# Kernel optimization log

Hardware: AMD Instinct MI355X
Metric: run time of the kernel (lower is better)

Reference implementation:

```python
import jax, jax.numpy as jnp
import numpy as np

B, S, D, H = 2, 2048, 1024, 16
DK = D // H
ROPE_BASE = 10000.0


def _rope_tables(seq_len, dim):
    # [S, dim] cos/sin tables, matching torch cat([freqs, freqs], -1)
    inv_freq = 1.0 / (ROPE_BASE ** (jnp.arange(0, dim, 2, dtype=jnp.float32) / dim))
    freqs = jnp.arange(seq_len, dtype=jnp.float32)[:, None] * inv_freq[None, :]
    emb = jnp.concatenate([freqs, freqs], axis=-1)
    return jnp.cos(emb), jnp.sin(emb)


def _rotate_half(x):
    x1, x2 = x[..., : x.shape[-1] // 2], x[..., x.shape[-1] // 2 :]
    return jnp.concatenate([-x2, x1], axis=-1)


def setup_inputs() -> dict:
    key = jax.random.key(0)
    ks = jax.random.split(key, 8)
    q = jax.random.normal(ks[0], (B, S, D), jnp.float32)
    k = jax.random.normal(ks[1], (B, S, D), jnp.float32)
    v = jax.random.normal(ks[2], (B, S, D), jnp.float32)
    mask = jnp.tril(jnp.ones((S, S), jnp.int32))[None, None]  # causal [1,1,S,S]
    scale = 0.02
    Wq = jax.random.normal(ks[3], (D, D), jnp.float32) * scale
    Wk = jax.random.normal(ks[4], (D, D), jnp.float32) * scale
    Wv = jax.random.normal(ks[5], (D, D), jnp.float32) * scale
    Wo = jax.random.normal(ks[6], (D, D), jnp.float32) * scale
    bq = jnp.zeros((D,), jnp.float32)
    bk = jnp.zeros((D,), jnp.float32)
    bv = jnp.zeros((D,), jnp.float32)
    bo = jnp.zeros((D,), jnp.float32)
    return {"q": q, "k": k, "v": v, "mask": mask,
            "Wq": Wq, "bq": bq, "Wk": Wk, "bk": bk,
            "Wv": Wv, "bv": bv, "Wo": Wo, "bo": bo}


def reference(q, k, v, mask, Wq, bq, Wk, bk, Wv, bv, Wo, bo):
    b, s, d = q.shape
    # QKV projections, reshape to [B, H, S, d_k]
    query = (q @ Wq + bq).reshape(b, s, H, DK).transpose(0, 2, 1, 3)
    key_ = (k @ Wk + bk).reshape(b, s, H, DK).transpose(0, 2, 1, 3)
    value = (v @ Wv + bv).reshape(b, s, H, DK).transpose(0, 2, 1, 3)
    # RoPE on q and k
    cos, sin = _rope_tables(s, DK)  # [S, DK]
    cos = cos[None, None]
    sin = sin[None, None]
    query = query * cos + _rotate_half(query) * sin
    key_ = key_ * cos + _rotate_half(key_) * sin
    # scaled dot-product attention with mask-fill
    scores = jnp.einsum("bhqd,bhkd->bhqk", query, key_) / jnp.sqrt(jnp.float32(DK))
    scores = jnp.where(mask == 0, jnp.float32(-1e9), scores)
    attn = jax.nn.softmax(scores, axis=-1)
    out = jnp.einsum("bhqk,bhkd->bhqd", attn, value)  # [B,H,S,DK]
    out = out.transpose(0, 2, 1, 3).reshape(b, s, d)
    return out @ Wo + bo
```

## Files before the change

### kernel.cpp

```cpp
#include <hip/hip_runtime.h>
#include <hip/hip_bf16.h>
#include <math.h>

#define Bb 2
#define Ss 2048
#define Dd 1024
#define Hh 16
#define DKk 64
#define BSn (Bb*Ss)

typedef unsigned short u16;
typedef __attribute__((ext_vector_type(8))) short frag_ab;
typedef __attribute__((ext_vector_type(4))) float frag_cd;

static __device__ __forceinline__ u16 f2bf(float x) {
    __hip_bfloat16 h = __float2bfloat16(x);
    return *reinterpret_cast<u16*>(&h);
}

static __device__ __forceinline__ void gload16(const u16* g, u16* l) {
    __builtin_amdgcn_global_load_lds(
        (const __attribute__((address_space(1))) void*)g,
        (__attribute__((address_space(3))) void*)l, 16, 0, 0);
}

__global__ __launch_bounds__(256)
void convert_kernel(const float* __restrict__ q, const float* __restrict__ k,
                    const float* __restrict__ v,
                    const float* __restrict__ Wq, const float* __restrict__ Wk,
                    const float* __restrict__ Wv, const float* __restrict__ Wo,
                    u16* __restrict__ qb, u16* __restrict__ kb, u16* __restrict__ vb,
                    u16* __restrict__ wqt, u16* __restrict__ wkt,
                    u16* __restrict__ wvt, u16* __restrict__ wot)
{
    __shared__ u16 T[64 * 80];
    const int tid = threadIdx.x;
    const int bid = blockIdx.x;
    if (bid < 3072) {
        int t = bid >> 10;
        const float* src = (t == 0) ? q : (t == 1) ? k : v;
        u16* dst = (t == 0) ? qb : (t == 1) ? kb : vb;
        size_t base = (size_t)(bid & 1023) * 4096;
#pragma unroll
        for (int i = 0; i < 4; ++i) {
            size_t e = base + (size_t)(tid + i * 256) * 4;
            float4 xv = *(const float4*)(src + e);
            ushort4 o;
            o.x = f2bf(xv.x); o.y = f2bf(xv.y); o.z = f2bf(xv.z); o.w = f2bf(xv.w);
            *(ushort4*)(dst + e) = o;
        }
    } else {
        int wbid = bid - 3072;
        int w = wbid >> 8;
        const float* src = (w == 0) ? Wq : (w == 1) ? Wk : (w == 2) ? Wv : Wo;
        u16* dst = (w == 0) ? wqt : (w == 1) ? wkt : (w == 2) ? wvt : wot;
        int t = wbid & 255;
        int k0 = (t >> 4) * 64, nt0 = (t & 15) * 64;
#pragma unroll
        for (int i = 0; i < 4; ++i) {
            int f = tid + i * 256;
            int kk = f >> 4, nn = (f & 15) * 4;
            float4 xv = *(const float4*)(src + (size_t)(k0 + kk) * Dd + nt0 + nn);
            T[(nn + 0) * 80 + kk] = f2bf(xv.x);
            T[(nn + 1) * 80 + kk] = f2bf(xv.y);
            T[(nn + 2) * 80 + kk] = f2bf(xv.z);
            T[(nn + 3) * 80 + kk] = f2bf(xv.w);
        }
        __syncthreads();
#pragma unroll
        for (int i = 0; i < 2; ++i) {
            int g = tid + i * 256;
            int nn = g >> 3, k8 = (g & 7) * 8;
            *(uint4*)(dst + (size_t)(nt0 + nn) * Dd + k0 + k8) =
                *(const uint4*)&T[nn * 80 + k8];
        }
    }
}

__global__ __launch_bounds__(256)
void gemm_bf16(const u16* __restrict__ X0, const u16* __restrict__ X1,
               const u16* __restrict__ X2,
               const u16* __restrict__ W0, const u16* __restrict__ W1,
               const u16* __restrict__ W2,
               const float* __restrict__ b0, const float* __restrict__ b1,
               const float* __restrict__ b2,
               u16* __restrict__ O0, u16* __restrict__ O1, u16* __restrict__ O2,
               float* __restrict__ OutF, int fused)
{
    __shared__ u16 As[128 * 64];
    __shared__ u16 Bs[64 * 64];

    const int tid = threadIdx.x;
    const int wv = tid >> 6, lane = tid & 63, l16 = lane & 15, quad = lane >> 4;
    const int n0 = blockIdx.x * 64, m0 = blockIdx.y * 128;
    const int z = blockIdx.z;

    const u16* X      = fused ? ((z == 0) ? X0 : (z == 1) ? X1 : X2) : X0;
    const u16* Wt     = fused ? ((z == 0) ? W0 : (z == 1) ? W1 : W2) : W0;
    const float* bias = fused ? ((z == 0) ? b0 : (z == 1) ? b1 : b2) : b0;
    u16* OutB         = (z == 0) ? O0 : (z == 1) ? O1 : O2;
    const int mode    = fused ? ((z == 0) ? 1 : (z == 1) ? 3 : 2) : 0;

    const int srow = tid >> 3;
    const int scol = (tid & 7) * 8;

    frag_cd acc[2][4];
#pragma unroll
    for (int ms = 0; ms < 2; ++ms)
#pragma unroll
        for (int n = 0; n < 4; ++n) acc[ms][n] = (frag_cd){0.f, 0.f, 0.f, 0.f};

    for (int k0 = 0; k0 < Dd; k0 += 64) {
        __syncthreads();
#pragma unroll
        for (int p = 0; p < 4; ++p)
            gload16(&X[(size_t)(m0 + p * 32 + srow) * Dd + k0 + scol],
                    &As[p * 2048 + wv * 512]);
#pragma unroll
        for (int p = 0; p < 2; ++p)
            gload16(&Wt[(size_t)(n0 + p * 32 + srow) * Dd + k0 + scol],
                    &Bs[p * 2048 + wv * 512]);
        __syncthreads();

#pragma unroll
        for (int ks = 0; ks < 2; ++ks) {
            frag_ab a0 = *(const frag_ab*)&As[(wv * 32 + l16) * 64 + ks * 32 + quad * 8];
            frag_ab a1 = *(const frag_ab*)&As[(wv * 32 + 16 + l16) * 64 + ks * 32 + quad * 8];
#pragma unroll
            for (int n = 0; n < 4; ++n) {
                frag_ab b = *(const frag_ab*)&Bs[(n * 16 + l16) * 64 + ks * 32 + quad * 8];
                acc[0][n] = __builtin_amdgcn_mfma_f32_16x16x32_bf16(a0, b, acc[0][n], 0, 0, 0);
                acc[1][n] = __builtin_amdgcn_mfma_f32_16x16x32_bf16(a1, b, acc[1][n], 0, 0, 0);
            }
        }
    }

    float bv4[4];
#pragma unroll
    for (int n = 0; n < 4; ++n) bv4[n] = bias[n0 + n * 16 + l16];

    if (mode == 0) {
#pragma unroll
        for (int ms = 0; ms < 2; ++ms)
#pragma unroll
            for (int r = 0; r < 4; ++r) {
                int row = m0 + wv * 32 + ms * 16 + quad * 4 + r;
#pragma unroll
                for (int n = 0; n < 4; ++n)
                    OutF[(size_t)row * Dd + n0 + n * 16 + l16] = acc[ms][n][r] + bv4[n];
            }
    } else if (mode == 2) {
        const int h = n0 >> 6;
        const int b = m0 >> 11;
#pragma unroll
        for (int ms = 0; ms < 2; ++ms) {
            int sbase = (m0 & (Ss - 1)) + wv * 32 + ms * 16 + quad * 4;
#pragma unroll
            for (int n = 0; n < 4; ++n) {
                int d = n * 16 + l16;
                ushort4 o;
                o.x = f2bf(acc[ms][n][0] + bv4[n]);
                o.y = f2bf(acc[ms][n][1] + bv4[n]);
                o.z = f2bf(acc[ms][n][2] + bv4[n]);
                o.w = f2bf(acc[ms][n][3] + bv4[n]);
                *(ushort4*)&OutB[(((size_t)b * Hh + h) * DKk + d) * Ss + sbase] = o;
            }
        }
    } else {
        const int h = n0 >> 6;
        const float lg = 0.28782313662425575f;
        const float sc = (mode == 1) ? 0.125f : 1.0f;
#pragma unroll
        for (int ms = 0; ms < 2; ++ms)
#pragma unroll
            for (int r = 0; r < 4; ++r) {
                int row = m0 + wv * 32 + ms * 16 + quad * 4 + r;
                int b = row >> 11, s = row & (Ss - 1);
                u16* orow = OutB + (((size_t)b * Hh + h) * Ss + s) * DKk;
#pragma unroll
                for (int n = 0; n < 2; ++n) {
                    int j = n * 16 + l16;
                    float ang = (float)s * __expf(-(float)j * lg);
                    float cv = cosf(ang), sv = sinf(ang);
                    float lo = acc[ms][n][r] + bv4[n];
                    float hi = acc[ms][n + 2][r] + bv4[n + 2];
                    orow[j]      = f2bf((lo * cv - hi * sv) * sc);
                    orow[j + 32] = f2bf((hi * cv + lo * sv) * sc);
                }
            }
    }
}

__global__ __launch_bounds__(256)
void attn_mfma(const u16* __restrict__ Q, const u16* __restrict__ K,
               const u16* __restrict__ Vt, u16* __restrict__ Aout)
{
    __shared__ u16 Qs[64 * 72];
    __shared__ u16 Ks[64 * 64];
    __shared__ u16 Vs[64 * 64];
    __shared__ u16 Ps[64 * 72];

    const int tid = threadIdx.x;
    const int wv = tid >> 6;
    const int lane = tid & 63;
    const int l16 = lane & 15;
    const int quad = lane >> 4;

    const int bh = blockIdx.y;
    const int vsw = (blockIdx.x + (bh & 7)) & 31;
    const int jj  = bh >> 3;
    const int qb  = (jj == 0) ? vsw
                  : (jj == 1) ? ((vsw + 8) & 31)
                  : (jj == 2) ? ((23 - vsw) & 31)
                  :             (31 - vsw);
    const int q0 = qb * 64;

    const size_t qkbase = (size_t)bh * Ss * DKk;
    const size_t vbase  = (size_t)bh * DKk * Ss;
    const int b = bh >> 4, h = bh & 15;

    const int srow = tid >> 3;
    const int scol = ((tid & 7) ^ (srow & 7)) * 8;
    const int sx   = (l16 & 7) * 8;

#pragma unroll
    for (int rep = 0; rep < 2; ++rep) {
        int g = tid + rep * 256;
        int row = g >> 3, c8 = (g & 7) * 8;
        *(uint4*)&Qs[row * 72 + c8] =
            *(const uint4*)&Q[qkbase + (size_t)(q0 + row) * DKk + c8];
    }

    float m_r[4], l_r[4];
#pragma unroll
    for (int r = 0; r < 4; ++r) { m_r[r] = -3.0e38f; l_r[r] = 0.f; }
    frag_cd of[4];
#pragma unroll
    for (int n = 0; n < 4; ++n) of[n] = (frag_cd){0.f, 0.f, 0.f, 0.f};

    for (int kb = 0; kb <= qb; ++kb) {
        const int k0 = kb * 64;
        __syncthreads();
#pragma unroll
        for (int p = 0; p < 2; ++p) {
            gload16(&K[qkbase + (size_t)(k0 + p * 32 + srow) * DKk + scol],
                    &Ks[p * 2048 + wv * 512]);
            gload16(&Vt[vbase + (size_t)(p * 32 + srow) * Ss + k0 + scol],
                    &Vs[p * 2048 + wv * 512]);
        }
        __syncthreads();

        frag_cd sf[4];
#pragma unroll
        for (int n = 0; n < 4; ++n) sf[n] = (frag_cd){0.f, 0.f, 0.f, 0.f};
#pragma unroll
        for (int h2 = 0; h2 < 2; ++h2) {
            frag_ab qa = *(const frag_ab*)&Qs[(wv * 16 + l16) * 72 + h2 * 32 + quad * 8];
#pragma unroll
            for (int n = 0; n < 4; ++n) {
                frag_ab kf = *(const frag_ab*)&Ks[(n * 16 + l16) * 64 + ((h2 * 32 + quad * 8) ^ sx)];
                sf[n] = __builtin_amdgcn_mfma_f32_16x16x32_bf16(qa, kf, sf[n], 0, 0, 0);
            }
        }

        if (kb == qb) {
#pragma unroll
            for (int r = 0; r < 4; ++r) {
                int qi = wv * 16 + quad * 4 + r;
#pragma unroll
                for (int n = 0; n < 4; ++n)
                    if (n * 16 + l16 > qi) sf[n][r] = -1.0e30f;
            }
        }

        float alpha[4];
#pragma unroll
        for (int r = 0; r < 4; ++r) {
            float mx = m_r[r];
#pragma unroll
            for (int n = 0; n < 4; ++n) mx = fmaxf(mx, sf[n][r]);
#pragma unroll
            for (int off = 1; off < 16; off <<= 1) mx = fmaxf(mx, __shfl_xor(mx, off));
            float a = __expf(m_r[r] - mx);
            m_r[r] = mx;
            float sum = 0.f;
#pragma unroll
            for (int n = 0; n < 4; ++n) {
                float p = __expf(sf[n][r] - mx);
                sf[n][r] = p;
                sum += p;
            }
#pragma unroll
            for (int off = 1; off < 16; off <<= 1) sum += __shfl_xor(sum, off);
            l_r[r] = l_r[r] * a + sum;
            alpha[r] = a;
        }
#pragma unroll
        for (int n = 0; n < 4; ++n)
#pragma unroll
            for (int r = 0; r < 4; ++r) of[n][r] *= alpha[r];

#pragma unroll
        for (int n = 0; n < 4; ++n)
#pragma unroll
            for (int r = 0; r < 4; ++r)
                Ps[(wv * 16 + quad * 4 + r) * 72 + n * 16 + l16] = f2bf(sf[n][r]);
        __threadfence_block();

#pragma unroll
        for (int h2 = 0; h2 < 2; ++h2) {
            frag_ab pa = *(const frag_ab*)&Ps[(wv * 16 + l16) * 72 + h2 * 32 + quad * 8];
#pragma unroll
            for (int n = 0; n < 4; ++n) {
                frag_ab vf = *(const frag_ab*)&Vs[(n * 16 + l16) * 64 + ((h2 * 32 + quad * 8) ^ sx)];
                of[n] = __builtin_amdgcn_mfma_f32_16x16x32_bf16(pa, vf, of[n], 0, 0, 0);
            }
        }
    }

#pragma unroll
    for (int r = 0; r < 4; ++r) {
        float inv = 1.f / l_r[r];
        int row = q0 + wv * 16 + quad * 4 + r;
        u16* orow = Aout + ((size_t)b * Ss + row) * Dd + h * DKk;
#pragma unroll
        for (int n = 0; n < 4; ++n) orow[n * 16 + l16] = f2bf(of[n][r] * inv);
    }
}

extern "C" void kernel_launch(void* const* d_in, const int* in_sizes, int n_in,
                              void* d_out, int out_size, void* d_ws, size_t ws_size,
                              hipStream_t stream) {
    (void)in_sizes; (void)n_in; (void)out_size;
    const float* q  = (const float*)d_in[0];
    const float* k  = (const float*)d_in[1];
    const float* v  = (const float*)d_in[2];
    const float* Wq = (const float*)d_in[4];
    const float* bq = (const float*)d_in[5];
    const float* Wk = (const float*)d_in[6];
    const float* bk = (const float*)d_in[7];
    const float* Wv = (const float*)d_in[8];
    const float* bv = (const float*)d_in[9];
    const float* Wo = (const float*)d_in[10];
    const float* bo = (const float*)d_in[11];
    float* out = (float*)d_out;

    const size_t E = (size_t)Bb * Ss * Dd;
    const size_t Wn = (size_t)Dd * Dd;
    const size_t need = (7 * E + 4 * Wn) * sizeof(u16);
    if (ws_size < need) return;
    u16* qa  = (u16*)d_ws;
    u16* ka  = qa + E;
    u16* va  = ka + E;
    u16* wqt = va + E;
    u16* wkt = wqt + Wn;
    u16* wvt = wkt + Wn;
    u16* wot = wvt + Wn;
    u16* Qh  = wot + Wn;
    u16* Kh  = Qh + E;
    u16* Vth = Kh + E;
    u16* Abf = Vth + E;

    convert_kernel<<<4096, 256, 0, stream>>>(q, k, v, Wq, Wk, Wv, Wo,
                                             qa, ka, va, wqt, wkt, wvt, wot);
    gemm_bf16<<<dim3(Dd / 64, BSn / 128, 3), 256, 0, stream>>>(
        qa, ka, va, wqt, wkt, wvt, bq, bk, bv, Qh, Kh, Vth, nullptr, 1);
    attn_mfma<<<dim3(32, Bb * Hh), 256, 0, stream>>>(Qh, Kh, Vth, Abf);
    gemm_bf16<<<dim3(Dd / 64, BSn / 128, 1), 256, 0, stream>>>(
        Abf, nullptr, nullptr, wot, nullptr, nullptr, bo, nullptr, nullptr,
        nullptr, nullptr, nullptr, out, 0);
}
```

Before: 274.1 us.

## Use exp2 softmax with lazy rescaling and XOR-swizzled Q/P tiles

Folds log2(e) into the Q scaling so the softmax can use exp2f instead of __expf. It also skips the running-max rescale of the output and row sum unless some row's max grows by more than 8 (in log2 units). The Q tile is now loaded with async global-to-LDS loads into an XOR-swizzled layout, and the P tile is stored with the same swizzle instead of row padding. Together these cut exp and multiply work and LDS bank conflicts. The lazy rescale lets probabilities exceed 1 by up to 2^8 before bf16 rounding, which is a small precision risk.

```diff
diff --git a/kernel.cpp b/kernel.cpp
--- a/kernel.cpp
+++ b/kernel.cpp
@@ -169,7 +169,7 @@
     } else {
         const int h = n0 >> 6;
         const float lg = 0.28782313662425575f;
-        const float sc = (mode == 1) ? 0.125f : 1.0f;
+        const float sc = (mode == 1) ? 0.18033688011112042f : 1.0f;
 #pragma unroll
         for (int ms = 0; ms < 2; ++ms)
 #pragma unroll
@@ -195,10 +195,10 @@
 void attn_mfma(const u16* __restrict__ Q, const u16* __restrict__ K,
                const u16* __restrict__ Vt, u16* __restrict__ Aout)
 {
-    __shared__ u16 Qs[64 * 72];
+    __shared__ u16 Qs[64 * 64];
     __shared__ u16 Ks[64 * 64];
     __shared__ u16 Vs[64 * 64];
-    __shared__ u16 Ps[64 * 72];
+    __shared__ u16 Ps[64 * 64];
 
     const int tid = threadIdx.x;
     const int wv = tid >> 6;
@@ -224,12 +224,9 @@
     const int sx   = (l16 & 7) * 8;
 
 #pragma unroll
-    for (int rep = 0; rep < 2; ++rep) {
-        int g = tid + rep * 256;
-        int row = g >> 3, c8 = (g & 7) * 8;
-        *(uint4*)&Qs[row * 72 + c8] =
-            *(const uint4*)&Q[qkbase + (size_t)(q0 + row) * DKk + c8];
-    }
+    for (int p = 0; p < 2; ++p)
+        gload16(&Q[qkbase + (size_t)(q0 + p * 32 + srow) * DKk + scol],
+                &Qs[p * 2048 + wv * 512]);
 
     float m_r[4], l_r[4];
 #pragma unroll
@@ -255,7 +252,7 @@
         for (int n = 0; n < 4; ++n) sf[n] = (frag_cd){0.f, 0.f, 0.f, 0.f};
 #pragma unroll
         for (int h2 = 0; h2 < 2; ++h2) {
-            frag_ab qa = *(const frag_ab*)&Qs[(wv * 16 + l16) * 72 + h2 * 32 + quad * 8];
+            frag_ab qa = *(const frag_ab*)&Qs[(wv * 16 + l16) * 64 + ((h2 * 32 + quad * 8) ^ sx)];
 #pragma unroll
             for (int n = 0; n < 4; ++n) {
                 frag_ab kf = *(const frag_ab*)&Ks[(n * 16 + l16) * 64 + ((h2 * 32 + quad * 8) ^ sx)];
@@ -273,7 +270,8 @@
             }
         }
 
-        float alpha[4];
+        float mx4[4];
+        bool need = false;
 #pragma unroll
         for (int r = 0; r < 4; ++r) {
             float mx = m_r[r];
@@ -281,35 +279,45 @@
             for (int n = 0; n < 4; ++n) mx = fmaxf(mx, sf[n][r]);
 #pragma unroll
             for (int off = 1; off < 16; off <<= 1) mx = fmaxf(mx, __shfl_xor(mx, off));
-            float a = __expf(m_r[r] - mx);
-            m_r[r] = mx;
+            mx4[r] = mx;
+            need = need || (mx > m_r[r] + 8.0f);
+        }
+        if (__any(need)) {
+#pragma unroll
+            for (int r = 0; r < 4; ++r) {
+                float a = exp2f(m_r[r] - mx4[r]);
+                m_r[r] = mx4[r];
+                l_r[r] *= a;
+#pragma unroll
+                for (int n = 0; n < 4; ++n) of[n][r] *= a;
+            }
+        }
+#pragma unroll
+        for (int r = 0; r < 4; ++r) {
             float sum = 0.f;
 #pragma unroll
             for (int n = 0; n < 4; ++n) {
-                float p = __expf(sf[n][r] - mx);
+                float p = exp2f(sf[n][r] - m_r[r]);
                 sf[n][r] = p;
                 sum += p;
             }
 #pragma unroll
             for (int off = 1; off < 16; off <<= 1) sum += __shfl_xor(sum, off);
-            l_r[r] = l_r[r] * a + sum;
-            alpha[r] = a;
-        }
+            l_r[r] += sum;
+        }
+
 #pragma unroll
         for (int n = 0; n < 4; ++n)
 #pragma unroll
-            for (int r = 0; r < 4; ++r) of[n][r] *= alpha[r];
-
-#pragma unroll
-        for (int n = 0; n < 4; ++n)
-#pragma unroll
-            for (int r = 0; r < 4; ++r)
-                Ps[(wv * 16 + quad * 4 + r) * 72 + n * 16 + l16] = f2bf(sf[n][r]);
+            for (int r = 0; r < 4; ++r) {
+                int row = wv * 16 + quad * 4 + r;
+                Ps[row * 64 + ((n * 16 + l16) ^ ((row & 7) << 3))] = f2bf(sf[n][r]);
+            }
         __threadfence_block();
 
 #pragma unroll
         for (int h2 = 0; h2 < 2; ++h2) {
-            frag_ab pa = *(const frag_ab*)&Ps[(wv * 16 + l16) * 72 + h2 * 32 + quad * 8];
+            frag_ab pa = *(const frag_ab*)&Ps[(wv * 16 + l16) * 64 + ((h2 * 32 + quad * 8) ^ sx)];
 #pragma unroll
             for (int n = 0; n < 4; ++n) {
                 frag_ab vf = *(const frag_ab*)&Vs[(n * 16 + l16) * 64 + ((h2 * 32 + quad * 8) ^ sx)];
```

After: 280.0 us. +2.1%, slower.
